# Optimization experiments

Hardware: AMD Instinct MI355X
Metric: run time of the kernel (lower is better)

Reference implementation:

```python
import jax, jax.numpy as jnp
import numpy as np

NEG = -9e15

def setup_inputs() -> dict:
    key = jax.random.key(0)
    k1, k2, k3, k4, k5, k6 = jax.random.split(key, 6)
    N, Fin, Fout = 8192, 256, 128
    inp = jax.random.normal(k1, (N, Fin), dtype=jnp.float32)
    adj = jax.random.randint(k2, (N, N), 0, 2, dtype=jnp.int32)
    W_w = jax.random.normal(k3, (Fout, Fin), dtype=jnp.float32) / np.sqrt(Fin)
    W_b = jax.random.normal(k4, (Fout,), dtype=jnp.float32) * 0.01
    a_w = jax.random.normal(k5, (1, 2 * Fout), dtype=jnp.float32) / np.sqrt(2 * Fout)
    a_b = jax.random.normal(k6, (1,), dtype=jnp.float32) * 0.01
    return {"input": inp, "adj": adj, "W_w": W_w, "W_b": W_b, "a_w": a_w, "a_b": a_b}

def reference(input, adj, W_w, W_b, a_w, a_b):
    alpha = 0.2
    Fout = W_w.shape[0]
    h = input @ W_w.T + W_b                      # [N, Fout]
    # a([h_i || h_j]) = a1.h_i + a2.h_j + b  (exact decomposition of concat+linear)
    a1 = a_w[0, :Fout]
    a2 = a_w[0, Fout:]
    e = jax.nn.leaky_relu((h @ a1)[:, None] + (h @ a2)[None, :] + a_b[0],
                          negative_slope=alpha)   # [N, N]
    scores = jnp.where(adj > 0, e, NEG)
    attention = jax.nn.softmax(scores, axis=1)    # dropout in eval mode = identity
    h_prime = attention @ h                       # [N, Fout]
    return jax.nn.elu(h_prime)
```

## Files before the change

kernel.cpp:

```cpp
#include <hip/hip_runtime.h>
#include <hip/hip_bf16.h>
#include <cmath>

#define NN 8192
#define FIN 256
#define FOUT 128
#define ROWS 32
#define NCH 4
#define JC (NN / NCH)
#define JSPAN (JC / 4)
#define NWIN (JSPAN / 64)

typedef short short8 __attribute__((ext_vector_type(8)));
typedef float f32x16 __attribute__((ext_vector_type(16)));
typedef unsigned long long u64;

static __device__ __forceinline__ unsigned short f2bf(float f) {
    unsigned u = __float_as_uint(f);
    u += 0x7fffu + ((u >> 16) & 1u);
    return (unsigned short)(u >> 16);
}

__global__ __launch_bounds__(256, 2)
void gat_pass_a(const float* __restrict__ input, const float* __restrict__ W,
                const float* __restrict__ Wb, const float* __restrict__ aw,
                const float* __restrict__ ab, unsigned short* __restrict__ hT3,
                float* __restrict__ s_out, float* __restrict__ t_out) {
    const int tid = threadIdx.x;
    const int w = tid >> 6, l = tid & 63;
    const int l5 = l >> 5, l31 = l & 31;
    const int nt = w >> 1, mh = w & 1;
    const int bx = blockIdx.x;
    const int i = bx * 64 + nt * 32 + l31;

    f32x16 acc0 = {}; f32x16 acc1 = {};
    #pragma unroll
    for (int ks = 0; ks < FIN / 16; ++ks) {
        const int c0 = ks * 16 + l5 * 8;
        const float4 b0 = *(const float4*)(input + (size_t)i * FIN + c0);
        const float4 b1 = *(const float4*)(input + (size_t)i * FIN + c0 + 4);
        short8 bf;
        bf[0]=(short)f2bf(b0.x); bf[1]=(short)f2bf(b0.y); bf[2]=(short)f2bf(b0.z); bf[3]=(short)f2bf(b0.w);
        bf[4]=(short)f2bf(b1.x); bf[5]=(short)f2bf(b1.y); bf[6]=(short)f2bf(b1.z); bf[7]=(short)f2bf(b1.w);
        {
            const int kcol = l31 + 32 * (2 * mh + 0);
            const float4 a0 = *(const float4*)(W + (size_t)kcol * FIN + c0);
            const float4 a1 = *(const float4*)(W + (size_t)kcol * FIN + c0 + 4);
            short8 af;
            af[0]=(short)f2bf(a0.x); af[1]=(short)f2bf(a0.y); af[2]=(short)f2bf(a0.z); af[3]=(short)f2bf(a0.w);
            af[4]=(short)f2bf(a1.x); af[5]=(short)f2bf(a1.y); af[6]=(short)f2bf(a1.z); af[7]=(short)f2bf(a1.w);
            acc0 = __builtin_amdgcn_mfma_f32_32x32x16_bf16(af, bf, acc0, 0, 0, 0);
        }
        {
            const int kcol = l31 + 32 * (2 * mh + 1);
            const float4 a0 = *(const float4*)(W + (size_t)kcol * FIN + c0);
            const float4 a1 = *(const float4*)(W + (size_t)kcol * FIN + c0 + 4);
            short8 af;
            af[0]=(short)f2bf(a0.x); af[1]=(short)f2bf(a0.y); af[2]=(short)f2bf(a0.z); af[3]=(short)f2bf(a0.w);
            af[4]=(short)f2bf(a1.x); af[5]=(short)f2bf(a1.y); af[6]=(short)f2bf(a1.z); af[7]=(short)f2bf(a1.w);
            acc1 = __builtin_amdgcn_mfma_f32_32x32x16_bf16(af, bf, acc1, 0, 0, 0);
        }
    }
    __shared__ float sred[4][32];
    __shared__ float tred[4][32];
    float sacc = 0.f, tacc = 0.f;
    const int jloc = nt * 32 + l31;
    const int ksb = jloc >> 4;
    const int lane_j = 32 * ((jloc >> 3) & 1);
    const int e = jloc & 7;
    #pragma unroll
    for (int m = 0; m < 2; ++m) {
        #pragma unroll
        for (int r = 0; r < 16; ++r) {
            const int kcol = 32 * (2 * mh + m) + 4 * l5 + (r & 3) + 8 * (r >> 2);
            const float hv = (m ? acc1[r] : acc0[r]) + Wb[kcol];
            const int fg = kcol >> 5;
            const int lane = (kcol & 31) + lane_j;
            hT3[((((size_t)bx * 4 + fg) * 4 + ksb) * 64 + lane) * 8 + e] = f2bf(hv);
            sacc += hv * aw[kcol];
            tacc += hv * aw[FOUT + kcol];
        }
    }
    sacc += __shfl_xor(sacc, 32);
    tacc += __shfl_xor(tacc, 32);
    if (l < 32) { sred[w][l] = sacc; tred[w][l] = tacc; }
    __syncthreads();
    if (mh == 0 && l < 32) {
        s_out[i] = sred[w][l] + sred[w + 1][l];
        t_out[i] = tred[w][l] + tred[w + 1][l] + ab[0];
    }
}

__global__ __launch_bounds__(256, 3)
void gat_pass_b(const int* __restrict__ adj, const unsigned short* __restrict__ hT3,
                const float* __restrict__ s_in, const float* __restrict__ t_in,
                float* __restrict__ numw, float* __restrict__ dpart) {
    __shared__ float red[FOUT * ROWS];
    __shared__ float denb[4][ROWS];
    __shared__ u64 mbuf[4][2][ROWS];
    const int tid = threadIdx.x;
    const int wv = tid >> 6, l = tid & 63;
    const int l5 = l >> 5, l31 = l & 31;
    const int i0 = blockIdx.x * ROWS;
    const int chunk = blockIdx.y;
    const int jwv = chunk * JC + wv * JSPAN;
    const float si = s_in[i0 + l31];

    const int* ab = adj + (size_t)(i0 + (l >> 4)) * NN + (l & 15) * 4 + jwv;
    u64* mb = &mbuf[wv][0][0];

    f32x16 acc0 = {}, acc1 = {}, acc2 = {}, acc3 = {};
    float dacc = 0.f;

    int4 R[8];
    const int kk = l & 3;
    const int sh = 16 * kk;
    const int lq = l >> 2;

    #define PACKQ(q, buf)                                                        \
    {                                                                            \
        const int4 a = R[q];                                                     \
        const u64 b0 = __ballot(a.x > 0);                                        \
        const u64 b1 = __ballot(a.y > 0);                                        \
        const u64 b2 = __ballot(a.z > 0);                                        \
        const u64 b3 = __ballot(a.w > 0);                                        \
        const u64 v = ((b0 >> sh) & 0xFFFFull) | (((b1 >> sh) & 0xFFFFull) << 16)\
                    | (((b2 >> sh) & 0xFFFFull) << 32)                           \
                    | (((b3 >> sh) & 0xFFFFull) << 48);                          \
        if (lq == (q)) mb[(buf) * ROWS + (q) * 4 + kk] = v;                      \
    }

    #pragma unroll
    for (int q = 0; q < 8; ++q) R[q] = *(const int4*)(ab + (size_t)q * 4 * NN);
    #pragma unroll
    for (int q = 0; q < 8; ++q) PACKQ(q, 0)
    __builtin_amdgcn_wave_barrier();

    for (int w = 0; w < NWIN; ++w) {
        const u64 myw = mb[(w & 1) * ROWS + l31];
        if (w + 1 < NWIN) {
            #pragma unroll
            for (int q = 0; q < 8; ++q)
                R[q] = *(const int4*)(ab + (size_t)q * 4 * NN + (w + 1) * 64);
        }
        const int tile = (jwv + w * 64) >> 6;
        #pragma unroll
        for (int ks = 0; ks < 4; ++ks) {
            const int jsl = jwv + w * 64 + ks * 16 + l5 * 8;
            const float4 t0 = *(const float4*)(t_in + jsl);
            const float4 t1 = *(const float4*)(t_in + jsl + 4);
            const u64 m = myw >> (ks * 4 + l5 * 2);
            short8 bf;
            float x, p;
            x = si + t0.x; x = fmaxf(x, 0.2f * x); p = __expf(x);
            p = ((m >> 0)  & 1ull) ? p : 0.f; dacc += p; bf[0] = (short)f2bf(p);
            x = si + t0.y; x = fmaxf(x, 0.2f * x); p = __expf(x);
            p = ((m >> 16) & 1ull) ? p : 0.f; dacc += p; bf[1] = (short)f2bf(p);
            x = si + t0.z; x = fmaxf(x, 0.2f * x); p = __expf(x);
            p = ((m >> 32) & 1ull) ? p : 0.f; dacc += p; bf[2] = (short)f2bf(p);
            x = si + t0.w; x = fmaxf(x, 0.2f * x); p = __expf(x);
            p = ((m >> 48) & 1ull) ? p : 0.f; dacc += p; bf[3] = (short)f2bf(p);
            x = si + t1.x; x = fmaxf(x, 0.2f * x); p = __expf(x);
            p = ((m >> 1)  & 1ull) ? p : 0.f; dacc += p; bf[4] = (short)f2bf(p);
            x = si + t1.y; x = fmaxf(x, 0.2f * x); p = __expf(x);
            p = ((m >> 17) & 1ull) ? p : 0.f; dacc += p; bf[5] = (short)f2bf(p);
            x = si + t1.z; x = fmaxf(x, 0.2f * x); p = __expf(x);
            p = ((m >> 33) & 1ull) ? p : 0.f; dacc += p; bf[6] = (short)f2bf(p);
            x = si + t1.w; x = fmaxf(x, 0.2f * x); p = __expf(x);
            p = ((m >> 49) & 1ull) ? p : 0.f; dacc += p; bf[7] = (short)f2bf(p);

            const unsigned short* hp =
                hT3 + (((size_t)tile * 4) * 4 + ks) * 512 + (size_t)l * 8;
            const short8 af0 = *(const short8*)(hp);
            const short8 af1 = *(const short8*)(hp + 2048);
            const short8 af2 = *(const short8*)(hp + 4096);
            const short8 af3 = *(const short8*)(hp + 6144);
            acc0 = __builtin_amdgcn_mfma_f32_32x32x16_bf16(af0, bf, acc0, 0, 0, 0);
            acc1 = __builtin_amdgcn_mfma_f32_32x32x16_bf16(af1, bf, acc1, 0, 0, 0);
            acc2 = __builtin_amdgcn_mfma_f32_32x32x16_bf16(af2, bf, acc2, 0, 0, 0);
            acc3 = __builtin_amdgcn_mfma_f32_32x32x16_bf16(af3, bf, acc3, 0, 0, 0);
        }
        if (w + 1 < NWIN) {
            #pragma unroll
            for (int q = 0; q < 8; ++q) PACKQ(q, (w + 1) & 1)
        }
        __builtin_amdgcn_wave_barrier();
    }
    #undef PACKQ

    #pragma unroll
    for (int ph = 0; ph < 4; ++ph) {
        __syncthreads();
        if (wv == ph) {
            #pragma unroll
            for (int r = 0; r < 16; ++r) {
                const int fr = (r & 3) + 8 * (r >> 2) + 4 * l5;
                if (ph == 0) {
                    red[(fr     ) * ROWS + l31] = acc0[r];
                    red[(fr + 32) * ROWS + l31] = acc1[r];
                    red[(fr + 64) * ROWS + l31] = acc2[r];
                    red[(fr + 96) * ROWS + l31] = acc3[r];
                } else {
                    red[(fr     ) * ROWS + l31] += acc0[r];
                    red[(fr + 32) * ROWS + l31] += acc1[r];
                    red[(fr + 64) * ROWS + l31] += acc2[r];
                    red[(fr + 96) * ROWS + l31] += acc3[r];
                }
            }
        }
    }
    dacc += __shfl_xor(dacc, 32);
    if (l5 == 0) denb[wv][l31] = dacc;
    __syncthreads();

    float* nb = numw + (size_t)chunk * FOUT * NN;
    #pragma unroll
    for (int e = 0; e < 4; ++e) {
        const int f = e * 32 + (tid >> 3);
        const int io = (tid & 7) * 4;
        *(float4*)(nb + (size_t)f * NN + i0 + io) = *(const float4*)(red + f * ROWS + io);
    }
    if (tid < ROWS)
        dpart[(size_t)chunk * NN + i0 + tid] =
            denb[0][tid] + denb[1][tid] + denb[2][tid] + denb[3][tid];
}

__global__ __launch_bounds__(256)
void gat_reduce(const float* __restrict__ numw, const float* __restrict__ dpart,
                float* __restrict__ out, int nchunk) {
    __shared__ float tile[FOUT * 33];
    __shared__ float dent[32];
    const int t = threadIdx.x;
    const int i0 = blockIdx.x * 32;
    if (t < 32) {
        float d = 0.f;
        for (int c = 0; c < nchunk; ++c) d += dpart[(size_t)c * NN + i0 + t];
        dent[t] = d;
    }
    __syncthreads();
    #pragma unroll
    for (int e = 0; e < 4; ++e) {
        const int f = e * 32 + (t >> 3);
        const int io = (t & 7) * 4;
        float4 s = {0.f, 0.f, 0.f, 0.f};
        for (int c = 0; c < nchunk; ++c) {
            const float4 v = *(const float4*)(numw + ((size_t)c * FOUT + f) * NN + i0 + io);
            s.x += v.x; s.y += v.y; s.z += v.z; s.w += v.w;
        }
        float v;
        v = s.x / dent[io + 0]; tile[f * 33 + io + 0] = (v > 0.f) ? v : expm1f(v);
        v = s.y / dent[io + 1]; tile[f * 33 + io + 1] = (v > 0.f) ? v : expm1f(v);
        v = s.z / dent[io + 2]; tile[f * 33 + io + 2] = (v > 0.f) ? v : expm1f(v);
        v = s.w / dent[io + 3]; tile[f * 33 + io + 3] = (v > 0.f) ? v : expm1f(v);
    }
    __syncthreads();
    #pragma unroll
    for (int e = 0; e < 4; ++e) {
        const int row = (t >> 5) * 4 + e;
        const int fo = (t & 31) * 4;
        const float4 v = { tile[(fo + 0) * 33 + row], tile[(fo + 1) * 33 + row],
                           tile[(fo + 2) * 33 + row], tile[(fo + 3) * 33 + row] };
        *(float4*)(out + (size_t)(i0 + row) * FOUT + fo) = v;
    }
}

extern "C" void kernel_launch(void* const* d_in, const int* in_sizes, int n_in,
                              void* d_out, int out_size, void* d_ws, size_t ws_size,
                              hipStream_t stream) {
    const float* input = (const float*)d_in[0];
    const int*   adj   = (const int*)d_in[1];
    const float* Ww    = (const float*)d_in[2];
    const float* Wb    = (const float*)d_in[3];
    const float* aw    = (const float*)d_in[4];
    const float* ab    = (const float*)d_in[5];
    float* out = (float*)d_out;

    char* ws = (char*)d_ws;
    unsigned short* hT3 = (unsigned short*)ws;
    float* s_buf = (float*)(ws + (size_t)FOUT * NN * 2);
    float* t_buf = s_buf + NN;
    float* dpart = t_buf + NN;
    float* numw = dpart + (size_t)NCH * NN;

    gat_pass_a<<<dim3(NN / 64), 256, 0, stream>>>(input, Ww, Wb, aw, ab, hT3, s_buf, t_buf);
    gat_pass_b<<<dim3(NN / ROWS, NCH), 256, 0, stream>>>(adj, hT3, s_buf, t_buf, numw, dpart);
    gat_reduce<<<dim3(NN / 32), 256, 0, stream>>>(numw, dpart, out, NCH);
}
```

Before: 115.5 us.

## Prepack adjacency bitmask for whole block upfront with row-contiguous loads

Pass B now has each wave load 8 full adjacency rows for the block's 2048-column chunk, with lanes reading contiguous 1KB spans. It packs them into a shared 32x33 u64 mask table before the compute loop, replacing the per-window double-buffered ballot packing interleaved with the MFMA work. Row-contiguous loads are meant to improve coalescing, and dropping the in-loop register buffering should free VGPRs, so launch bounds rise to 4 blocks per SM. The cost is that adjacency loading is no longer overlapped with exp/MFMA compute, and a block-wide barrier is added before the main loop.

```diff
diff --git a/kernel.cpp b/kernel.cpp
--- a/kernel.cpp
+++ b/kernel.cpp
@@ -8,8 +8,8 @@
 #define ROWS 32
 #define NCH 4
 #define JC (NN / NCH)
-#define JSPAN (JC / 4)
-#define NWIN (JSPAN / 64)
+#define NWINC (JC / 64)
+#define NWIN 8
 
 typedef short short8 __attribute__((ext_vector_type(8)));
 typedef float f32x16 __attribute__((ext_vector_type(16)));
@@ -91,62 +91,64 @@
     }
 }
 
-__global__ __launch_bounds__(256, 3)
+__global__ __launch_bounds__(256, 4)
 void gat_pass_b(const int* __restrict__ adj, const unsigned short* __restrict__ hT3,
                 const float* __restrict__ s_in, const float* __restrict__ t_in,
                 float* __restrict__ numw, float* __restrict__ dpart) {
     __shared__ float red[FOUT * ROWS];
     __shared__ float denb[4][ROWS];
-    __shared__ u64 mbuf[4][2][ROWS];
+    __shared__ u64 mask[ROWS][33];
     const int tid = threadIdx.x;
     const int wv = tid >> 6, l = tid & 63;
     const int l5 = l >> 5, l31 = l & 31;
     const int i0 = blockIdx.x * ROWS;
     const int chunk = blockIdx.y;
-    const int jwv = chunk * JC + wv * JSPAN;
+    const int jb = chunk * JC;
     const float si = s_in[i0 + l31];
 
-    const int* ab = adj + (size_t)(i0 + (l >> 4)) * NN + (l & 15) * 4 + jwv;
-    u64* mb = &mbuf[wv][0][0];
+    const int* arow = adj + (size_t)(i0 + wv * 8) * NN + jb + l * 4;
+    const int lq = (l & 31) >> 2;
+    const int sh = 16 * (l & 3);
+    int4 Rc[8];
+    #pragma unroll
+    for (int q = 0; q < 8; ++q) Rc[q] = *(const int4*)(arow + q * 256);
+    #pragma unroll
+    for (int rr = 0; rr < 8; ++rr) {
+        u64 myword = 0;
+        #pragma unroll
+        for (int q = 0; q < 8; ++q) {
+            const int4 a = Rc[q];
+            const u64 b0 = __ballot(a.x > 0);
+            const u64 b1 = __ballot(a.y > 0);
+            const u64 b2 = __ballot(a.z > 0);
+            const u64 b3 = __ballot(a.w > 0);
+            if (lq == q) {
+                myword = ((b0 >> sh) & 0xFFFFull)
+                       | (((b1 >> sh) & 0xFFFFull) << 16)
+                       | (((b2 >> sh) & 0xFFFFull) << 32)
+                       | (((b3 >> sh) & 0xFFFFull) << 48);
+            }
+        }
+        if (rr < 7) {
+            #pragma unroll
+            for (int q = 0; q < 8; ++q)
+                Rc[q] = *(const int4*)(arow + (size_t)(rr + 1) * NN + q * 256);
+        }
+        if (l < 32) mask[wv * 8 + rr][l] = myword;
+    }
+    __syncthreads();
 
     f32x16 acc0 = {}, acc1 = {}, acc2 = {}, acc3 = {};
     float dacc = 0.f;
 
-    int4 R[8];
-    const int kk = l & 3;
-    const int sh = 16 * kk;
-    const int lq = l >> 2;
-
-    #define PACKQ(q, buf)                                                        \
-    {                                                                            \
-        const int4 a = R[q];                                                     \
-        const u64 b0 = __ballot(a.x > 0);                                        \
-        const u64 b1 = __ballot(a.y > 0);                                        \
-        const u64 b2 = __ballot(a.z > 0);                                        \
-        const u64 b3 = __ballot(a.w > 0);                                        \
-        const u64 v = ((b0 >> sh) & 0xFFFFull) | (((b1 >> sh) & 0xFFFFull) << 16)\
-                    | (((b2 >> sh) & 0xFFFFull) << 32)                           \
-                    | (((b3 >> sh) & 0xFFFFull) << 48);                          \
-        if (lq == (q)) mb[(buf) * ROWS + (q) * 4 + kk] = v;                      \
-    }
-
-    #pragma unroll
-    for (int q = 0; q < 8; ++q) R[q] = *(const int4*)(ab + (size_t)q * 4 * NN);
-    #pragma unroll
-    for (int q = 0; q < 8; ++q) PACKQ(q, 0)
-    __builtin_amdgcn_wave_barrier();
-
     for (int w = 0; w < NWIN; ++w) {
-        const u64 myw = mb[(w & 1) * ROWS + l31];
-        if (w + 1 < NWIN) {
-            #pragma unroll
-            for (int q = 0; q < 8; ++q)
-                R[q] = *(const int4*)(ab + (size_t)q * 4 * NN + (w + 1) * 64);
-        }
-        const int tile = (jwv + w * 64) >> 6;
+        const int win = wv * NWIN + w;
+        const u64 myw = mask[l31][win];
+        const int jw = jb + win * 64;
+        const int tile = jw >> 6;
         #pragma unroll
         for (int ks = 0; ks < 4; ++ks) {
-            const int jsl = jwv + w * 64 + ks * 16 + l5 * 8;
+            const int jsl = jw + ks * 16 + l5 * 8;
             const float4 t0 = *(const float4*)(t_in + jsl);
             const float4 t1 = *(const float4*)(t_in + jsl + 4);
             const u64 m = myw >> (ks * 4 + l5 * 2);
@@ -180,13 +182,7 @@
             acc2 = __builtin_amdgcn_mfma_f32_32x32x16_bf16(af2, bf, acc2, 0, 0, 0);
             acc3 = __builtin_amdgcn_mfma_f32_32x32x16_bf16(af3, bf, acc3, 0, 0, 0);
         }
-        if (w + 1 < NWIN) {
-            #pragma unroll
-            for (int q = 0; q < 8; ++q) PACKQ(q, (w + 1) & 1)
-        }
-        __builtin_amdgcn_wave_barrier();
-    }
-    #undef PACKQ
+    }
 
     #pragma unroll
     for (int ph = 0; ph < 4; ++ph) {
```

Result: faster. 106.1 us (-8.1%).
